# Optimization experiments

Hardware: AMD Instinct MI355X
Metric: run time of the kernel (lower is better)

The kernel has to match this reference:

```python
import jax, jax.numpy as jnp
import numpy as np

WIN = 7


def rel_index(win: int) -> jnp.ndarray:
    ys, xs = jnp.meshgrid(jnp.arange(win), jnp.arange(win), indexing='ij')
    coords = jnp.stack([ys.reshape(-1), xs.reshape(-1)], axis=-1)  # (S, 2)
    diff = coords[None, :, :] - coords[:, None, :] + (win - 1)     # (S, S, 2)
    return diff[..., 0] * (2 * win - 1) + diff[..., 1]             # (S, S)


def setup_inputs() -> dict:
    key = jax.random.key(0)
    ks = jax.random.split(key, 5)
    B, WN, S, C, H = 64, 64, WIN * WIN, 192, 6
    X = jax.random.normal(ks[0], (B, WN, S, C), dtype=jnp.float32)
    # torch nn.Linear(emb_dim, 3*emb_dim) -> store as (in, out) for x @ W
    Wqkv = jax.random.normal(ks[1], (C, 3 * C), dtype=jnp.float32) * 0.02
    bqkv = jnp.zeros((3 * C,), dtype=jnp.float32)
    Wo = jax.random.normal(ks[2], (C, C), dtype=jnp.float32) * 0.02
    bo = jnp.zeros((C,), dtype=jnp.float32)
    bias_table = jax.random.normal(ks[3], ((2 * WIN - 1) ** 2, H), dtype=jnp.float32) * 0.02
    return {"X": X, "Wqkv": Wqkv, "bqkv": bqkv, "Wo": Wo, "bo": bo, "bias_table": bias_table}


def reference(X, Wqkv, bqkv, Wo, bo, bias_table):
    B, WN, S, C = X.shape
    H = bias_table.shape[1]
    D = C // H
    scale = D ** -0.5
    # qkv projection: (B, WN, S, 3C) -> (3, B, WN, H, S, D)
    qkv = (X @ Wqkv + bqkv).reshape(B, WN, S, 3, H, D).transpose(3, 0, 1, 4, 2, 5)
    q, k, v = qkv[0], qkv[1], qkv[2]
    attn = jnp.einsum('bwhqd,bwhkd->bwhqk', q, k) * scale  # (B, WN, H, S, S)
    # gathered relative position bias: (S, S, H) -> (H, S, S)
    idx = rel_index(WIN)
    bias = bias_table[idx].transpose(2, 0, 1)
    attn = attn + bias[None, None]
    proba = jax.nn.softmax(attn, axis=-1)  # dropout omitted (eval mode)
    out = jnp.einsum('bwhqk,bwhkd->bwhqd', proba, v)  # (B, WN, H, S, D)
    out = out.transpose(0, 1, 3, 2, 4).reshape(B, WN, S, C)
    return out @ Wo + bo
```

## Files before the change

kernel.cpp:

```cpp
#include <hip/hip_runtime.h>
#include <hip/hip_bf16.h>


typedef __attribute__((ext_vector_type(4))) float f32x4;
typedef __attribute__((ext_vector_type(8))) short bf16x8;
typedef __attribute__((ext_vector_type(4))) unsigned short u16x4;

#define SCALE 0.17677669529663689f
#define MFMA(a, b, acc) __builtin_amdgcn_mfma_f32_16x16x32_bf16(a, b, acc, 0, 0, 0)

__device__ __forceinline__ unsigned short f2bf(float f) {
  union { float f; unsigned int u; } v; v.f = f;
  return (unsigned short)((v.u + 0x7FFFu + ((v.u >> 16) & 1u)) >> 16);
}

__device__ __forceinline__ void gll16(const unsigned short* src, unsigned short* dst) {
  __builtin_amdgcn_global_load_lds(
      (const __attribute__((address_space(1))) unsigned int*)src,
      (__attribute__((address_space(3))) unsigned int*)dst, 16, 0, 0);
}

__global__ void wprep(const float* __restrict__ Wqkv, const float* __restrict__ Wo,
                      unsigned short* __restrict__ WqkvTs, unsigned short* __restrict__ WoTs) {
  int i = blockIdx.x * 256 + threadIdx.x;
  if (i < 576 * 192) {
    int n = i / 192, k = i % 192;
    int ch = n >> 6, row = n & 63;
    int dst = ch * 12288 + row * 192 + (((k >> 3) ^ (row & 7)) << 3) + (k & 7);
    WqkvTs[dst] = f2bf(Wqkv[k * 576 + n]);
  }
  if (i < 192 * 192) {
    int n = i / 192, k = i % 192;
    int dst = n * 192 + (((k >> 3) ^ (n & 7)) << 3) + (k & 7);
    WoTs[dst] = f2bf(Wo[k * 192 + n]);
  }
}

__global__ __launch_bounds__(512, 4)
void qkv_gemm(const float* __restrict__ X, const unsigned short* __restrict__ WqkvTs,
              const float* __restrict__ bqkv, unsigned short* __restrict__ qkv) {
  __shared__ __align__(16) unsigned short Bs[2][12288];
  __shared__ __align__(16) unsigned short scr[8][1152];
  __shared__ float biasLds[576];

  const int tid = threadIdx.x, w8 = tid >> 6, lane = tid & 63;
  const int g = lane >> 4, c = lane & 15;
  const size_t bm = (size_t)blockIdx.x * 128;
  const f32x4 z = {0.f, 0.f, 0.f, 0.f};

  #pragma unroll
  for (int jj = 0; jj < 3; ++jj)
    gll16(WqkvTs + (w8 * 3 + jj) * 512 + lane * 8, &Bs[0][(w8 * 3 + jj) * 512]);
  for (int j = tid; j < 576; j += 512) biasLds[j] = bqkv[j];

  bf16x8 af[6];
  {
    const float* xr = X + (bm + w8 * 16 + c) * 192;
    #pragma unroll
    for (int ks = 0; ks < 6; ++ks) {
      f32x4 lo = *(const f32x4*)(xr + ks * 32 + g * 8);
      f32x4 hi = *(const f32x4*)(xr + ks * 32 + g * 8 + 4);
      bf16x8 a;
      a[0] = (short)f2bf(lo[0]); a[1] = (short)f2bf(lo[1]);
      a[2] = (short)f2bf(lo[2]); a[3] = (short)f2bf(lo[3]);
      a[4] = (short)f2bf(hi[0]); a[5] = (short)f2bf(hi[1]);
      a[6] = (short)f2bf(hi[2]); a[7] = (short)f2bf(hi[3]);
      af[ks] = a;
    }
  }
  asm volatile("s_waitcnt vmcnt(0)\n\ts_barrier" ::: "memory");
  __builtin_amdgcn_sched_barrier(0);

  unsigned short* sw = scr[w8];
  for (int nc = 0; nc < 9; ++nc) {
    const int cur = nc & 1;
    if (nc < 8) {
      #pragma unroll
      for (int jj = 0; jj < 3; ++jj)
        gll16(WqkvTs + (nc + 1) * 12288 + (w8 * 3 + jj) * 512 + lane * 8,
              &Bs[cur ^ 1][(w8 * 3 + jj) * 512]);
    }
    f32x4 acc[4] = {z, z, z, z};
    #pragma unroll
    for (int ks = 0; ks < 6; ++ks) {
      #pragma unroll
      for (int nf = 0; nf < 4; ++nf) {
        const bf16x8 bv = *(const bf16x8*)(
            &Bs[cur][(nf * 16 + c) * 192 + (((ks * 4 + g) ^ (c & 7)) << 3)]);
        acc[nf] = MFMA(af[ks], bv, acc[nf]);
      }
    }
    #pragma unroll
    for (int nf = 0; nf < 4; ++nf) {
      const float bb = biasLds[nc * 64 + nf * 16 + c];
      #pragma unroll
      for (int r = 0; r < 4; ++r)
        sw[(4 * g + r) * 72 + nf * 16 + c] = f2bf(acc[nf][r] + bb);
    }
    uint4 o0 = *(const uint4*)(sw + c * 72 + g * 8);
    uint4 o1 = *(const uint4*)(sw + c * 72 + 32 + g * 8);
    unsigned short* qp = qkv + (bm + w8 * 16 + c) * 576 + nc * 64;
    *(uint4*)(qp + g * 8)      = o0;
    *(uint4*)(qp + 32 + g * 8) = o1;

    if (nc < 8) {
      asm volatile("s_waitcnt vmcnt(2)\n\ts_barrier" ::: "memory");
      __builtin_amdgcn_sched_barrier(0);
    }
  }
}

__global__ __launch_bounds__(512, 4)
void attn_win(unsigned short* __restrict__ qkv, const float* __restrict__ btab) {
  __shared__ __align__(16) unsigned short Ks[64 * 200];
  __shared__ __align__(16) unsigned short Vt[192 * 72];
  __shared__ __align__(16) unsigned short scr[8][1152];
  __shared__ float biasF[1014];

  const int tid = threadIdx.x, w8 = tid >> 6, lane = tid & 63;
  const int g = lane >> 4, c = lane & 15;
  const int mt = w8 & 3, hw = w8 >> 2;
  const size_t tokbase = (size_t)blockIdx.x * 49;
  const f32x4 z = {0.f, 0.f, 0.f, 0.f};

  for (int j = tid; j < 1014; j += 512) biasF[j] = btab[j];
  for (int j = tid; j < 360; j += 512) {
    uint4 zz = {0, 0, 0, 0};
    *(uint4*)(&Ks[(49 + j / 24) * 200 + (j % 24) * 8]) = zz;
  }
  for (int j = tid; j < 2880; j += 512) Vt[(j / 15) * 72 + 49 + j % 15] = 0;
  for (int j = tid; j < 1176; j += 512) {
    int row = j / 24, ch = j % 24;
    *(uint4*)(&Ks[row * 200 + ch * 8]) =
        *(const uint4*)(qkv + (tokbase + row) * 576 + 192 + ch * 8);
  }
  for (int j = tid; j < 1176; j += 512) {
    int row = j / 24, ch = j % 24;
    uint4 v = *(const uint4*)(qkv + (tokbase + row) * 576 + 384 + ch * 8);
    const unsigned short* e = (const unsigned short*)&v;
    #pragma unroll
    for (int m = 0; m < 8; ++m) {
      int k = (ch + m) & 7;
      Vt[(ch * 8 + k) * 72 + row] = e[k];
    }
  }

  const int qbase = mt * 16;
  const int q = qbase + c;
  const bool qvalid = q < 49;
  const int qc = qvalid ? q : 48;

  bf16x8 bqh[3];
  #pragma unroll
  for (int hi = 0; hi < 3; ++hi)
    bqh[hi] = *(const bf16x8*)(qkv + (tokbase + qc) * 576 + (hw * 3 + hi) * 32 + g * 8);

  __syncthreads();

  const int qoff6 = ((6 - qc / 7) * 13 + (6 - qc % 7)) * 6;
  int kb6[16];
  #pragma unroll
  for (int i = 0; i < 16; ++i) {
    int k = (i >> 2) * 16 + g * 4 + (i & 3);
    int kk = k < 49 ? k : 48;
    kb6[i] = ((kk / 7) * 13 + (kk % 7)) * 6;
  }
  unsigned short* Pw = scr[w8];

  #pragma unroll
  for (int hi = 0; hi < 3; ++hi) {
    const int h = hw * 3 + hi;
    const bf16x8 bq = bqh[hi];
    const int cofs = h * 32 + g * 8;
    f32x4 s0 = MFMA(*(const bf16x8*)(Ks + (c) * 200 + cofs), bq, z);
    f32x4 s1 = MFMA(*(const bf16x8*)(Ks + (16 + c) * 200 + cofs), bq, z);
    f32x4 s2 = MFMA(*(const bf16x8*)(Ks + (32 + c) * 200 + cofs), bq, z);
    f32x4 s3 = MFMA(*(const bf16x8*)(Ks + (48 + c) * 200 + cofs), bq, z);

    float p[16];
    float mx = -3e38f;
    #pragma unroll
    for (int i = 0; i < 16; ++i) {
      const int t = i >> 2, r = i & 3;
      const int k = t * 16 + g * 4 + r;
      const float sv = (t == 0) ? s0[r] : (t == 1) ? s1[r] : (t == 2) ? s2[r] : s3[r];
      const float b = biasF[kb6[i] + qoff6 + h];
      const float lg = (qvalid && (k < 49)) ? fmaf(sv, SCALE, b) : -1e30f;
      p[i] = lg;
      mx = fmaxf(mx, lg);
    }
    mx = fmaxf(mx, __shfl_xor(mx, 16));
    mx = fmaxf(mx, __shfl_xor(mx, 32));
    float sum = 0.f;
    #pragma unroll
    for (int i = 0; i < 16; ++i) { p[i] = __expf(p[i] - mx); sum += p[i]; }
    sum += __shfl_xor(sum, 16);
    sum += __shfl_xor(sum, 32);
    const float inv = 1.0f / sum;
    #pragma unroll
    for (int t = 0; t < 4; ++t) {
      u16x4 pkv;
      #pragma unroll
      for (int r = 0; r < 4; ++r) pkv[r] = f2bf(p[t * 4 + r] * inv);
      *(u16x4*)(Pw + c * 72 + t * 16 + g * 4) = pkv;
    }

    f32x4 o0 = z, o1 = z;
    #pragma unroll
    for (int ks = 0; ks < 2; ++ks) {
      const bf16x8 ap = *(const bf16x8*)(Pw + c * 72 + ks * 32 + g * 8);
      const bf16x8 v0 = *(const bf16x8*)(Vt + (h * 32 + c) * 72 + ks * 32 + g * 8);
      const bf16x8 v1 = *(const bf16x8*)(Vt + (h * 32 + 16 + c) * 72 + ks * 32 + g * 8);
      o0 = MFMA(ap, v0, o0);
      o1 = MFMA(ap, v1, o1);
    }
    #pragma unroll
    for (int r = 0; r < 4; ++r) {
      Pw[(4 * g + r) * 72 + c]      = f2bf(o0[r]);
      Pw[(4 * g + r) * 72 + 16 + c] = f2bf(o1[r]);
    }
    uint4 ov = *(const uint4*)(Pw + c * 72 + g * 8);
    if (qvalid)
      *(uint4*)(qkv + (tokbase + q) * 576 + h * 32 + g * 8) = ov;
  }
}

__global__ __launch_bounds__(512, 4)
void out_gemm(const unsigned short* __restrict__ qkv, const unsigned short* __restrict__ WoTs,
              const float* __restrict__ bo, float* __restrict__ out) {
  __shared__ __align__(16) unsigned short Ws[192 * 192];

  const int tid = threadIdx.x, w8 = tid >> 6, lane = tid & 63;
  const int g = lane >> 4, c = lane & 15;
  const size_t bm = (size_t)blockIdx.x * 128;
  const f32x4 z = {0.f, 0.f, 0.f, 0.f};

  #pragma unroll
  for (int jj = 0; jj < 9; ++jj)
    gll16(WoTs + (w8 * 9 + jj) * 512 + lane * 8, &Ws[(w8 * 9 + jj) * 512]);

  bf16x8 af[6];
  #pragma unroll
  for (int ks = 0; ks < 6; ++ks)
    af[ks] = *(const bf16x8*)(qkv + (bm + w8 * 16 + c) * 576 + ks * 32 + g * 8);
  __syncthreads();

  #pragma unroll
  for (int nf = 0; nf < 12; ++nf) {
    const int col = nf * 16 + c;
    f32x4 acc = z;
    #pragma unroll
    for (int ks = 0; ks < 6; ++ks) {
      const bf16x8 bv = *(const bf16x8*)(
          &Ws[col * 192 + (((ks * 4 + g) ^ (c & 7)) << 3)]);
      acc = MFMA(af[ks], bv, acc);
    }
    const float bb = bo[col];
    #pragma unroll
    for (int r = 0; r < 4; ++r)
      out[(bm + w8 * 16 + 4 * g + r) * 192 + col] = acc[r] + bb;
  }
}

extern "C" void kernel_launch(void* const* d_in, const int* in_sizes, int n_in,
                              void* d_out, int out_size, void* d_ws, size_t ws_size,
                              hipStream_t stream) {
  (void)in_sizes; (void)n_in; (void)out_size; (void)ws_size;
  const float* X    = (const float*)d_in[0];
  const float* Wqkv = (const float*)d_in[1];
  const float* bqkv = (const float*)d_in[2];
  const float* Wo   = (const float*)d_in[3];
  const float* bo   = (const float*)d_in[4];
  const float* btab = (const float*)d_in[5];

  unsigned short* WqkvTs = (unsigned short*)d_ws;
  unsigned short* WoTs   = WqkvTs + 576 * 192;
  unsigned short* qkv    = WoTs + 192 * 192;

  wprep<<<432, 256, 0, stream>>>(Wqkv, Wo, WqkvTs, WoTs);
  qkv_gemm<<<1568, 512, 0, stream>>>(X, WqkvTs, bqkv, qkv);
  attn_win<<<4096, 512, 0, stream>>>(qkv, btab);
  out_gemm<<<1568, 512, 0, stream>>>(qkv, WoTs, bo, (float*)d_out);
}
```

Measured before the change: 281.4 us.

## Stream Wo from global in out_gemm, swap MFMA operands, vectorize V transpose

out_gemm no longer stages the full 192x192 Wo tile in LDS. It reads a plain-transposed Wo directly from global/L2 with the MFMA operands swapped, so each lane writes a contiguous float4 output with a vector bias add, and the block barrier goes away. Dropping the 72KB LDS buffer allows a higher launch-bounds occupancy target. In attn_win, the V transpose now loads four tokens at a time and writes 4-wide LDS stores, and the padding zeroing is consolidated, to cut scalar LDS store count. The trade-off is redundant global reads of Wo across waves.

```diff
diff --git a/kernel.cpp b/kernel.cpp
--- a/kernel.cpp
+++ b/kernel.cpp
@@ -21,7 +21,7 @@
 }
 
 __global__ void wprep(const float* __restrict__ Wqkv, const float* __restrict__ Wo,
-                      unsigned short* __restrict__ WqkvTs, unsigned short* __restrict__ WoTs) {
+                      unsigned short* __restrict__ WqkvTs, unsigned short* __restrict__ WoT) {
   int i = blockIdx.x * 256 + threadIdx.x;
   if (i < 576 * 192) {
     int n = i / 192, k = i % 192;
@@ -31,8 +31,7 @@
   }
   if (i < 192 * 192) {
     int n = i / 192, k = i % 192;
-    int dst = n * 192 + (((k >> 3) ^ (n & 7)) << 3) + (k & 7);
-    WoTs[dst] = f2bf(Wo[k * 192 + n]);
+    WoT[n * 192 + k] = f2bf(Wo[k * 192 + n]);
   }
 }
 
@@ -124,24 +123,45 @@
   const f32x4 z = {0.f, 0.f, 0.f, 0.f};
 
   for (int j = tid; j < 1014; j += 512) biasF[j] = btab[j];
-  for (int j = tid; j < 360; j += 512) {
-    uint4 zz = {0, 0, 0, 0};
-    *(uint4*)(&Ks[(49 + j / 24) * 200 + (j % 24) * 8]) = zz;
-  }
-  for (int j = tid; j < 2880; j += 512) Vt[(j / 15) * 72 + 49 + j % 15] = 0;
+  for (int j = tid; j < 192; j += 512) {
+    unsigned short* vd = Vt + j * 72;
+    const u16x4 z4 = {0, 0, 0, 0};
+    vd[49] = 0;
+    *(unsigned int*)(vd + 50) = 0u;
+    *(u16x4*)(vd + 52) = z4;
+    *(u16x4*)(vd + 56) = z4;
+    *(u16x4*)(vd + 60) = z4;
+  }
   for (int j = tid; j < 1176; j += 512) {
     int row = j / 24, ch = j % 24;
     *(uint4*)(&Ks[row * 200 + ch * 8]) =
         *(const uint4*)(qkv + (tokbase + row) * 576 + 192 + ch * 8);
   }
-  for (int j = tid; j < 1176; j += 512) {
-    int row = j / 24, ch = j % 24;
-    uint4 v = *(const uint4*)(qkv + (tokbase + row) * 576 + 384 + ch * 8);
-    const unsigned short* e = (const unsigned short*)&v;
+  for (int j = tid; j < 288; j += 512) {
+    int g4 = j / 24, ch = j % 24;
+    const unsigned short* vb = qkv + (tokbase + 4 * g4) * 576 + 384 + ch * 8;
+    uint4 v0 = *(const uint4*)(vb);
+    uint4 v1 = *(const uint4*)(vb + 576);
+    uint4 v2 = *(const uint4*)(vb + 1152);
+    uint4 v3 = *(const uint4*)(vb + 1728);
+    const unsigned short* e0 = (const unsigned short*)&v0;
+    const unsigned short* e1 = (const unsigned short*)&v1;
+    const unsigned short* e2 = (const unsigned short*)&v2;
+    const unsigned short* e3 = (const unsigned short*)&v3;
     #pragma unroll
     for (int m = 0; m < 8; ++m) {
       int k = (ch + m) & 7;
-      Vt[(ch * 8 + k) * 72 + row] = e[k];
+      u16x4 t; t[0] = e0[k]; t[1] = e1[k]; t[2] = e2[k]; t[3] = e3[k];
+      *(u16x4*)(&Vt[(ch * 8 + k) * 72 + 4 * g4]) = t;
+    }
+  }
+  for (int j = tid; j < 24; j += 512) {
+    uint4 v = *(const uint4*)(qkv + (tokbase + 48) * 576 + 384 + j * 8);
+    const unsigned short* e = (const unsigned short*)&v;
+    #pragma unroll
+    for (int m = 0; m < 8; ++m) {
+      int k = (j + m) & 7;
+      Vt[(j * 8 + k) * 72 + 48] = e[k];
     }
   }
 
@@ -225,40 +245,28 @@
   }
 }
 
-__global__ __launch_bounds__(512, 4)
-void out_gemm(const unsigned short* __restrict__ qkv, const unsigned short* __restrict__ WoTs,
+__global__ __launch_bounds__(512, 8)
+void out_gemm(const unsigned short* __restrict__ qkv, const unsigned short* __restrict__ WoT,
               const float* __restrict__ bo, float* __restrict__ out) {
-  __shared__ __align__(16) unsigned short Ws[192 * 192];
-
   const int tid = threadIdx.x, w8 = tid >> 6, lane = tid & 63;
   const int g = lane >> 4, c = lane & 15;
-  const size_t bm = (size_t)blockIdx.x * 128;
+  const size_t r0 = (size_t)blockIdx.x * 128 + w8 * 16;
   const f32x4 z = {0.f, 0.f, 0.f, 0.f};
 
-  #pragma unroll
-  for (int jj = 0; jj < 9; ++jj)
-    gll16(WoTs + (w8 * 9 + jj) * 512 + lane * 8, &Ws[(w8 * 9 + jj) * 512]);
-
   bf16x8 af[6];
   #pragma unroll
   for (int ks = 0; ks < 6; ++ks)
-    af[ks] = *(const bf16x8*)(qkv + (bm + w8 * 16 + c) * 576 + ks * 32 + g * 8);
-  __syncthreads();
+    af[ks] = *(const bf16x8*)(qkv + (r0 + c) * 576 + ks * 32 + g * 8);
 
   #pragma unroll
   for (int nf = 0; nf < 12; ++nf) {
-    const int col = nf * 16 + c;
     f32x4 acc = z;
-    #pragma unroll
-    for (int ks = 0; ks < 6; ++ks) {
-      const bf16x8 bv = *(const bf16x8*)(
-          &Ws[col * 192 + (((ks * 4 + g) ^ (c & 7)) << 3)]);
-      acc = MFMA(af[ks], bv, acc);
-    }
-    const float bb = bo[col];
-    #pragma unroll
-    for (int r = 0; r < 4; ++r)
-      out[(bm + w8 * 16 + 4 * g + r) * 192 + col] = acc[r] + bb;
+    const unsigned short* wr = WoT + (nf * 16 + c) * 192 + g * 8;
+    #pragma unroll
+    for (int ks = 0; ks < 6; ++ks)
+      acc = MFMA(*(const bf16x8*)(wr + ks * 32), af[ks], acc);
+    const f32x4 bb = *(const f32x4*)(bo + nf * 16 + 4 * g);
+    *(f32x4*)(out + (r0 + c) * 192 + nf * 16 + 4 * g) = acc + bb;
   }
 }
 
@@ -274,11 +282,11 @@
   const float* btab = (const float*)d_in[5];
 
   unsigned short* WqkvTs = (unsigned short*)d_ws;
-  unsigned short* WoTs   = WqkvTs + 576 * 192;
-  unsigned short* qkv    = WoTs + 192 * 192;
-
-  wprep<<<432, 256, 0, stream>>>(Wqkv, Wo, WqkvTs, WoTs);
+  unsigned short* WoT    = WqkvTs + 576 * 192;
+  unsigned short* qkv    = WoT + 192 * 192;
+
+  wprep<<<432, 256, 0, stream>>>(Wqkv, Wo, WqkvTs, WoT);
   qkv_gemm<<<1568, 512, 0, stream>>>(X, WqkvTs, bqkv, qkv);
   attn_win<<<4096, 512, 0, stream>>>(qkv, btab);
-  out_gemm<<<1568, 512, 0, stream>>>(qkv, WoTs, bo, (float*)d_out);
-}
+  out_gemm<<<1568, 512, 0, stream>>>(qkv, WoT, bo, (float*)d_out);
+}
```

After: 373.4 us. 1.33x slower.
